# Performance work log

Hardware: AMD Instinct MI355X
Metric: run time of the kernel (lower is better)

The kernel has to match this reference:

```python
import jax, jax.numpy as jnp
import numpy as np

HIDDEN = 1024
HEADS = 16
HEAD_DIM = HIDDEN // HEADS


def setup_inputs() -> dict:
    key = jax.random.key(0)
    ks = jax.random.split(key, 7)
    B, S, H = 8, 1024, HIDDEN
    hidden_states = jax.random.normal(ks[0], (B, S, H), dtype=jnp.float32)
    attention_mask = jnp.zeros((B, 1, 1, S), dtype=jnp.float32)
    # Xavier-uniform weights [out, in], zero biases (matches module init)
    limit = float(np.sqrt(6.0 / (H + H)))
    Wq = jax.random.uniform(ks[1], (H, H), minval=-limit, maxval=limit, dtype=jnp.float32)
    Wk = jax.random.uniform(ks[2], (H, H), minval=-limit, maxval=limit, dtype=jnp.float32)
    Wv = jax.random.uniform(ks[3], (H, H), minval=-limit, maxval=limit, dtype=jnp.float32)
    bq = jnp.zeros((H,), dtype=jnp.float32)
    bk = jnp.zeros((H,), dtype=jnp.float32)
    bv = jnp.zeros((H,), dtype=jnp.float32)
    return {"hidden_states": hidden_states, "attention_mask": attention_mask,
            "Wq": Wq, "bq": bq, "Wk": Wk, "bk": bk, "Wv": Wv, "bv": bv}


def _split_heads(x):
    # [B, S, H] -> [B, heads, S, head_dim]
    B, S, _ = x.shape
    return x.reshape(B, S, HEADS, HEAD_DIM).transpose(0, 2, 1, 3)


def reference(hidden_states, attention_mask, Wq, bq, Wk, bk, Wv, bv):
    # Linear projections: y = x @ W^T + b  (weights stored [out, in] as in torch)
    q = _split_heads(hidden_states @ Wq.T + bq)
    k = _split_heads(hidden_states @ Wk.T + bk)
    v = _split_heads(hidden_states @ Wv.T + bv)
    scale = 1.0 / (HEAD_DIM ** 0.5)
    scores = jnp.einsum('bhqd,bhkd->bhqk', q, k) * scale  # [B,heads,S,S]
    scores = scores + attention_mask
    probs = jax.nn.softmax(scores, axis=-1)
    # dropout is identity at inference
    ctx = jnp.einsum('bhqk,bhkd->bhqd', probs, v)
    B, _, S, _ = ctx.shape
    return ctx.transpose(0, 2, 1, 3).reshape(B, S, HIDDEN)
```

## Files before the change

### kernel.cpp

```cpp
#include <hip/hip_runtime.h>
#include <hip/hip_bf16.h>
#include <stdint.h>

#define B_ 8
#define S_ 1024
#define NH_ 16
#define D_ 64
#define H_ 1024
#define M_TOT (B_*S_)
#define LOG2E 1.44269504088896f

typedef __attribute__((ext_vector_type(8))) short short8;
typedef __attribute__((ext_vector_type(4))) float f32x4;
typedef __attribute__((ext_vector_type(16))) float f32x16;

#if __has_builtin(__builtin_amdgcn_exp2f)
#define EXP2(x) __builtin_amdgcn_exp2f(x)
#else
#define EXP2(x) __expf((x) * 0.69314718056f)
#endif

static __device__ __forceinline__ unsigned short f2bf(float f) {
  union { float f; unsigned u; } c; c.f = f;
  unsigned u = c.u;
  return (unsigned short)((u + 0x7fffu + ((u >> 16) & 1u)) >> 16);
}

static __device__ __forceinline__ void gld_lds16(void* lds, const void* g) {
  __builtin_amdgcn_global_load_lds((const __attribute__((address_space(1))) unsigned*)g,
                                   (__attribute__((address_space(3))) unsigned*)lds, 16, 0, 0);
}

__global__ void cvt_f32_bf16(const float* __restrict__ X,
                             const float* __restrict__ Wq,
                             const float* __restrict__ Wk,
                             const float* __restrict__ Wv,
                             unsigned short* __restrict__ Xbf,
                             unsigned short* __restrict__ Wbf) {
  const long long NX = (long long)M_TOT * H_;
  const long long NW = (long long)H_ * H_;
  long long t = (long long)blockIdx.x * blockDim.x + threadIdx.x;
  const long long stride = (long long)gridDim.x * blockDim.x;
  const long long total4 = (NX + 3 * NW) >> 2;
  for (; t < total4; t += stride) {
    long long e = t << 2;
    const float* src; unsigned short* dst;
    if (e < NX) { src = X + e; dst = Xbf + e; }
    else {
      long long r = e - NX;
      int w = (int)(r / NW);
      long long o = r - (long long)w * NW;
      src = (w == 0 ? Wq : (w == 1 ? Wk : Wv)) + o;
      dst = Wbf + (long long)w * NW + o;
    }
    float4 v = *(const float4*)src;
    ushort4 u;
    u.x = f2bf(v.x); u.y = f2bf(v.y); u.z = f2bf(v.z); u.w = f2bf(v.w);
    *(ushort4*)dst = u;
  }
}

#define GBM 128
#define GBN 128
#define GBK 64

__global__ __launch_bounds__(256) void qkv_gemm(
    const unsigned short* __restrict__ Xbf,
    const unsigned short* __restrict__ Wbf,
    const float* __restrict__ bq, const float* __restrict__ bk,
    const float* __restrict__ bv,
    unsigned short* __restrict__ Qo, unsigned short* __restrict__ Ko,
    unsigned short* __restrict__ Vt) {
  __shared__ char lds[GBM * GBK * 2 * 2];
  char* ldsA = lds;
  char* ldsB = lds + GBM * GBK * 2;

  const int tid = threadIdx.x;
  const int w = tid >> 6;
  const int l = tid & 63;
  const int z = blockIdx.z;
  const int mtile = blockIdx.x * GBM;
  const int ntile = blockIdx.y * GBN;
  const int wm = w >> 1, wn = w & 1;
  const int lrow = l & 15, lgrp = l >> 4;

  const unsigned short* Wz = Wbf + (long long)z * H_ * H_;

  f32x4 acc[4][4];
  f32x4 zero = {0.f, 0.f, 0.f, 0.f};
  #pragma unroll
  for (int i = 0; i < 4; ++i)
    #pragma unroll
    for (int j = 0; j < 4; ++j) acc[i][j] = zero;

  for (int kt = 0; kt < H_ / GBK; ++kt) {
    const int k0 = kt * GBK;
    #pragma unroll
    for (int t = 0; t < 4; ++t) {
      int j = w * 4 + t;
      int row = j * 8 + (l >> 3);
      int so = ((l & 7) ^ (row & 7)) * 8;
      gld_lds16(ldsA + j * 1024, Xbf + (long long)(mtile + row) * H_ + k0 + so);
      gld_lds16(ldsB + j * 1024, Wz  + (long long)(ntile + row) * H_ + k0 + so);
    }
    __syncthreads();

    char* srcA = (z == 2) ? ldsB : ldsA;
    char* srcB = (z == 2) ? ldsA : ldsB;
    const int wA = (z == 2) ? wn : wm;
    const int wB = (z == 2) ? wm : wn;

    short8 af[4][2], bf[4][2];
    #pragma unroll
    for (int ib = 0; ib < 4; ++ib)
      #pragma unroll
      for (int ks = 0; ks < 2; ++ks) {
        int rA = wA * 64 + ib * 16 + lrow;
        af[ib][ks] = *(const short8*)(srcA + rA * 128 + (((ks * 4 + lgrp) ^ (rA & 7)) * 16));
        int rB = wB * 64 + ib * 16 + lrow;
        bf[ib][ks] = *(const short8*)(srcB + rB * 128 + (((ks * 4 + lgrp) ^ (rB & 7)) * 16));
      }
    #pragma unroll
    for (int ib = 0; ib < 4; ++ib)
      #pragma unroll
      for (int jb = 0; jb < 4; ++jb)
        #pragma unroll
        for (int ks = 0; ks < 2; ++ks)
          acc[ib][jb] = __builtin_amdgcn_mfma_f32_16x16x32_bf16(
              af[ib][ks], bf[jb][ks], acc[ib][jb], 0, 0, 0);
    __syncthreads();
  }

  const float* bias = (z == 0) ? bq : (z == 1) ? bk : bv;
  if (z != 2) {
    unsigned short* O = (z == 0) ? Qo : Ko;
    #pragma unroll
    for (int jb = 0; jb < 4; ++jb) {
      int n = ntile + wn * 64 + jb * 16 + lrow;
      float bv_ = bias[n];
      int h = n >> 6, d = n & 63;
      #pragma unroll
      for (int ib = 0; ib < 4; ++ib)
        #pragma unroll
        for (int r = 0; r < 4; ++r) {
          int m = mtile + wm * 64 + ib * 16 + lgrp * 4 + r;
          float val = acc[ib][jb][r] + bv_;
          if (z == 0) val *= 0.125f * LOG2E;
          int b = m >> 10, s = m & 1023;
          O[(((long long)(b * NH_ + h)) * S_ + s) * D_ + d] = f2bf(val);
        }
    }
  } else {
    #pragma unroll
    for (int ib = 0; ib < 4; ++ib)
      #pragma unroll
      for (int r = 0; r < 4; ++r) {
        int n = ntile + wn * 64 + ib * 16 + lgrp * 4 + r;
        float bv_ = bias[n];
        int h = n >> 6, d = n & 63;
        #pragma unroll
        for (int jb = 0; jb < 4; ++jb) {
          int m = mtile + wm * 64 + jb * 16 + lrow;
          float val = acc[ib][jb][r] + bv_;
          int b = m >> 10, s = m & 1023;
          Vt[(((long long)(b * NH_ + h)) * D_ + d) * S_ + s] = f2bf(val);
        }
      }
  }
}

__global__ __launch_bounds__(256, 2) void attn_fused(
    const unsigned short* __restrict__ Qbf,
    const unsigned short* __restrict__ Kbf,
    const unsigned short* __restrict__ Vtb,
    const float* __restrict__ mask,
    float* __restrict__ out) {
  __shared__ char lds[32768];
  const int tid = threadIdx.x, w = tid >> 6, l = tid & 63;
  const int l31 = l & 31, h = l >> 5;

  const int lid = blockIdx.x;
  const int xcd = lid & 7, k8 = lid >> 3;
  const int bh = xcd * 16 + (k8 >> 2);
  const int qt = k8 & 3;
  const int b = bh >> 4, hd = bh & 15;
  const int q0 = qt * 256 + w * 64;

  const unsigned short* Kg = Kbf + (long long)bh * S_ * D_;
  const unsigned short* Vg = Vtb + (long long)bh * D_ * S_;
  const float* mrow = mask + b * S_;

  {
    const int row = (w * 2) * 8 + (l >> 3);
    const int row1 = (w * 2 + 1) * 8 + (l >> 3);
    const int so = ((l & 7) ^ (row & 7)) * 8;
    const int so1 = ((l & 7) ^ (row1 & 7)) * 8;
    gld_lds16(lds + (w * 2) * 1024,        Kg + (long long)row * D_ + so);
    gld_lds16(lds + (w * 2 + 1) * 1024,    Kg + (long long)row1 * D_ + so1);
    gld_lds16(lds + 8192 + (w * 2) * 1024, Vg + (long long)row * S_ + so);
    gld_lds16(lds + 8192 + (w * 2 + 1) * 1024, Vg + (long long)row1 * S_ + so1);
  }

  short8 qf[2][4];
  #pragma unroll
  for (int qb = 0; qb < 2; ++qb)
    #pragma unroll
    for (int ks = 0; ks < 4; ++ks)
      qf[qb][ks] = *(const short8*)(Qbf + ((long long)bh * S_ + q0 + qb * 32 + l31) * D_ + ks * 16 + 8 * h);

  f32x16 acc[2][2];
  #pragma unroll
  for (int db = 0; db < 2; ++db)
    #pragma unroll
    for (int qb = 0; qb < 2; ++qb)
      #pragma unroll
      for (int r = 0; r < 16; ++r) acc[db][qb][r] = 0.f;
  float m_run[2] = {-1e30f, -1e30f};
  float l_run[2] = {0.f, 0.f};

  __syncthreads();

  for (int kt = 0; kt < S_ / 64; ++kt) {
    const int p = kt & 1;
    char* ldsK = lds + p * 16384;
    char* ldsV = ldsK + 8192;
    const int key0 = kt * 64;

    if (kt < S_ / 64 - 1) {
      char* nb = lds + (p ^ 1) * 16384;
      const int nk0 = key0 + 64;
      #pragma unroll
      for (int t = 0; t < 2; ++t) {
        int j = w * 2 + t;
        int row = j * 8 + (l >> 3);
        int so = ((l & 7) ^ (row & 7)) * 8;
        gld_lds16(nb + j * 1024,        Kg + (long long)(nk0 + row) * D_ + so);
        gld_lds16(nb + 8192 + j * 1024, Vg + (long long)row * S_ + nk0 + so);
      }
    }

    f32x16 sc[2][2];
    #pragma unroll
    for (int kb = 0; kb < 2; ++kb)
      #pragma unroll
      for (int qb = 0; qb < 2; ++qb)
        #pragma unroll
        for (int r = 0; r < 16; ++r) sc[kb][qb][r] = 0.f;

    #pragma unroll
    for (int kb = 0; kb < 2; ++kb) {
      short8 kf[4];
      #pragma unroll
      for (int ks = 0; ks < 4; ++ks) {
        int row = kb * 32 + l31;
        int g = (2 * ks + h) ^ (row & 7);
        kf[ks] = *(const short8*)(ldsK + row * 128 + g * 16);
      }
      __builtin_amdgcn_s_setprio(1);
      #pragma unroll
      for (int qb = 0; qb < 2; ++qb)
        #pragma unroll
        for (int ks = 0; ks < 4; ++ks)
          sc[kb][qb] = __builtin_amdgcn_mfma_f32_32x32x16_bf16(
              kf[ks], qf[qb][ks], sc[kb][qb], 0, 0, 0);
      __builtin_amdgcn_s_setprio(0);
    }

    short8 pfrag[2][4];
    #pragma unroll
    for (int qb = 0; qb < 2; ++qb) {
      float sv[32];
      #pragma unroll
      for (int kb = 0; kb < 2; ++kb)
        #pragma unroll
        for (int rg = 0; rg < 4; ++rg) {
          f32x4 m4 = *(const f32x4*)(mrow + key0 + kb * 32 + rg * 8 + 4 * h);
          #pragma unroll
          for (int c = 0; c < 4; ++c)
            sv[kb * 16 + rg * 4 + c] = fmaf(m4[c], LOG2E, sc[kb][qb][rg * 4 + c]);
        }
      float r16[16];
      #pragma unroll
      for (int i = 0; i < 16; ++i) r16[i] = fmaxf(sv[i], sv[i + 16]);
      #pragma unroll
      for (int i = 0; i < 8; ++i) r16[i] = fmaxf(r16[i], r16[i + 8]);
      #pragma unroll
      for (int i = 0; i < 4; ++i) r16[i] = fmaxf(r16[i], r16[i + 4]);
      float pm = fmaxf(fmaxf(r16[0], r16[1]), fmaxf(r16[2], r16[3]));
      pm = fmaxf(pm, __shfl_xor(pm, 32));
      if (!__all(pm - m_run[qb] <= 11.5f)) {
        float mn = fmaxf(m_run[qb], pm);
        float rs = EXP2(m_run[qb] - mn);
        m_run[qb] = mn;
        l_run[qb] *= rs;
        #pragma unroll
        for (int db = 0; db < 2; ++db)
          #pragma unroll
          for (int r = 0; r < 16; ++r) acc[db][qb][r] *= rs;
      }
      const float mcur = m_run[qb];
      #pragma unroll
      for (int i = 0; i < 32; ++i) sv[i] = EXP2(sv[i] - mcur);
      #pragma unroll
      for (int i = 0; i < 16; ++i) r16[i] = sv[i] + sv[i + 16];
      #pragma unroll
      for (int i = 0; i < 8; ++i) r16[i] = r16[i] + r16[i + 8];
      #pragma unroll
      for (int i = 0; i < 4; ++i) r16[i] = r16[i] + r16[i + 4];
      float ps = (r16[0] + r16[1]) + (r16[2] + r16[3]);
      ps += __shfl_xor(ps, 32);
      l_run[qb] += ps;

      unsigned Wd[8][2];
      #pragma unroll
      for (int j = 0; j < 8; ++j) {
        int base = (j >> 2) * 16 + (j & 3) * 4;
        asm("v_cvt_pk_bf16_f32 %0, %1, %2" : "=v"(Wd[j][0]) : "v"(sv[base + 0]), "v"(sv[base + 1]));
        asm("v_cvt_pk_bf16_f32 %0, %1, %2" : "=v"(Wd[j][1]) : "v"(sv[base + 2]), "v"(sv[base + 3]));
      }
      #pragma unroll
      for (int ks = 0; ks < 4; ++ks) {
        unsigned s0 = h ? Wd[2 * ks][0] : Wd[2 * ks + 1][0];
        unsigned s1 = h ? Wd[2 * ks][1] : Wd[2 * ks + 1][1];
        unsigned r0 = __shfl_xor(s0, 32);
        unsigned r1 = __shfl_xor(s1, 32);
        unsigned o0 = h ? Wd[2 * ks + 1][0] : Wd[2 * ks][0];
        unsigned o1 = h ? Wd[2 * ks + 1][1] : Wd[2 * ks][1];
        union { unsigned u[4]; short8 s; } fu;
        fu.u[0] = h ? r0 : o0;
        fu.u[1] = h ? r1 : o1;
        fu.u[2] = h ? o0 : r0;
        fu.u[3] = h ? o1 : r1;
        pfrag[qb][ks] = fu.s;
      }
    }

    #pragma unroll
    for (int db = 0; db < 2; ++db) {
      short8 vf[4];
      #pragma unroll
      for (int ks = 0; ks < 4; ++ks) {
        int row = db * 32 + l31;
        int g = (2 * ks + h) ^ (row & 7);
        vf[ks] = *(const short8*)(ldsV + row * 128 + g * 16);
      }
      __builtin_amdgcn_s_setprio(1);
      #pragma unroll
      for (int qb = 0; qb < 2; ++qb)
        #pragma unroll
        for (int ks = 0; ks < 4; ++ks)
          acc[db][qb] = __builtin_amdgcn_mfma_f32_32x32x16_bf16(
              vf[ks], pfrag[qb][ks], acc[db][qb], 0, 0, 0);
      __builtin_amdgcn_s_setprio(0);
    }

    __syncthreads();
  }

  #pragma unroll
  for (int qb = 0; qb < 2; ++qb) {
    float inv = 1.0f / l_run[qb];
    int q = q0 + qb * 32 + l31;
    float* orow = out + ((long long)b * S_ + q) * H_ + hd * D_;
    #pragma unroll
    for (int db = 0; db < 2; ++db)
      #pragma unroll
      for (int rg = 0; rg < 4; ++rg) {
        f32x4 v4;
        #pragma unroll
        for (int c = 0; c < 4; ++c) v4[c] = acc[db][qb][rg * 4 + c] * inv;
        *(f32x4*)(orow + db * 32 + rg * 8 + 4 * h) = v4;
      }
  }
}

extern "C" void kernel_launch(void* const* d_in, const int* in_sizes, int n_in,
                              void* d_out, int out_size, void* d_ws, size_t ws_size,
                              hipStream_t stream) {
  const float* X    = (const float*)d_in[0];
  const float* mask = (const float*)d_in[1];
  const float* Wq   = (const float*)d_in[2];
  const float* bq   = (const float*)d_in[3];
  const float* Wk   = (const float*)d_in[4];
  const float* bk   = (const float*)d_in[5];
  const float* Wv   = (const float*)d_in[6];
  const float* bv   = (const float*)d_in[7];
  float* out = (float*)d_out;

  char* ws = (char*)d_ws;
  unsigned short* Xbf = (unsigned short*)ws;
  unsigned short* Wbf = (unsigned short*)(ws + 16777216);
  unsigned short* Qb  = (unsigned short*)(ws + 23068672);
  unsigned short* Kb  = (unsigned short*)(ws + 39845888);
  unsigned short* Vt  = (unsigned short*)(ws + 56623104);

  hipLaunchKernelGGL(cvt_f32_bf16, dim3(2048), dim3(256), 0, stream,
                     X, Wq, Wk, Wv, Xbf, Wbf);
  hipLaunchKernelGGL(qkv_gemm, dim3(M_TOT / GBM, H_ / GBN, 3), dim3(256), 0, stream,
                     Xbf, Wbf, bq, bk, bv, Qb, Kb, Vt);
  hipLaunchKernelGGL(attn_fused, dim3(512), dim3(256), 0, stream,
                     Qb, Kb, Vt, mask, out);
}
```

Baseline: 138.0 us.

## Rewrite QKV GEMM with 256x128 tiles, triple-buffered LDS pipeline and XCD-aware grid

The QKV projection GEMM now uses 512-thread blocks on 256x128 tiles. Global-to-LDS loads go through a three-stage ring buffer, so tile k+2 is fetched while tile k is computed, and each k-step is split into four MFMA quadrants with explicit barriers, waitcnts and setprio. The 1D grid is remapped so consecutive blocks on the same XCD share N/z tiles, aiming for better L2 reuse. The goal is to hide load latency and cut per-iteration syncthreads stalls, at the cost of 144KB of LDS, which limits occupancy, and fragile hand-written vmcnt counting.

```diff
diff --git a/kernel.cpp b/kernel.cpp
--- a/kernel.cpp
+++ b/kernel.cpp
@@ -30,6 +30,11 @@
   __builtin_amdgcn_global_load_lds((const __attribute__((address_space(1))) unsigned*)g,
                                    (__attribute__((address_space(3))) unsigned*)lds, 16, 0, 0);
 }
+
+#define WAIT_LGKM0() asm volatile("s_waitcnt lgkmcnt(0)" ::: "memory")
+#define WAIT_VM(n)   asm volatile("s_waitcnt vmcnt(" #n ")" ::: "memory")
+#define SBAR()       __builtin_amdgcn_s_barrier()
+#define SCHED0()     __builtin_amdgcn_sched_barrier(0)
 
 __global__ void cvt_f32_bf16(const float* __restrict__ X,
                              const float* __restrict__ Wq,
@@ -60,31 +65,60 @@
   }
 }
 
-#define GBM 128
-#define GBN 128
-#define GBK 64
-
-__global__ __launch_bounds__(256) void qkv_gemm(
+#define QBM 256
+#define QBN 128
+#define QBK 64
+#define BUFSZ 49152
+
+__global__ __launch_bounds__(512, 2) void qkv_gemm(
     const unsigned short* __restrict__ Xbf,
     const unsigned short* __restrict__ Wbf,
     const float* __restrict__ bq, const float* __restrict__ bk,
     const float* __restrict__ bv,
     unsigned short* __restrict__ Qo, unsigned short* __restrict__ Ko,
     unsigned short* __restrict__ Vt) {
-  __shared__ char lds[GBM * GBK * 2 * 2];
-  char* ldsA = lds;
-  char* ldsB = lds + GBM * GBK * 2;
+  __shared__ char lds[3 * BUFSZ];
 
   const int tid = threadIdx.x;
   const int w = tid >> 6;
   const int l = tid & 63;
-  const int z = blockIdx.z;
-  const int mtile = blockIdx.x * GBM;
-  const int ntile = blockIdx.y * GBN;
+  const int lrow = l & 15, lgrp = l >> 4;
   const int wm = w >> 1, wn = w & 1;
-  const int lrow = l & 15, lgrp = l >> 4;
+
+  const int orig = blockIdx.x;
+  const int id = (orig & 7) * 96 + (orig >> 3);
+  const int mtile = (id & 31) * QBM;
+  const int rest = id >> 5;
+  const int ntile = (rest & 7) * QBN;
+  const int z = rest >> 3;
 
   const unsigned short* Wz = Wbf + (long long)z * H_ * H_;
+
+  const int srow = l >> 3;
+  const int sslot = l & 7;
+  auto stageA = [&](char* buf, int j, int k0) {
+    int row = j * 8 + srow;
+    int so = (sslot ^ (row & 7)) * 8;
+    gld_lds16(buf + j * 1024, Xbf + (long long)(mtile + row) * H_ + k0 + so);
+  };
+  auto stageB = [&](char* buf, int j, int k0) {
+    int row = j * 8 + srow;
+    int so = (sslot ^ (row & 7)) * 8;
+    gld_lds16(buf + 32768 + j * 1024, Wz + (long long)(ntile + row) * H_ + k0 + so);
+  };
+
+  const int strA = (z == 2 ? wn : wm) * 64;
+  const int strB = (z == 2 ? wm : wn) * 64;
+  const int offA = (z == 2) ? 32768 : 0;
+  const int offB = (z == 2) ? 0 : 32768;
+  auto rdA = [&](char* buf, int mh, int sub, int ks) -> short8 {
+    int r = strA + mh * 32 + sub * 16 + lrow;
+    return *(const short8*)(buf + offA + r * 128 + (((ks * 4 + lgrp) ^ (r & 7)) * 16));
+  };
+  auto rdB = [&](char* buf, int nh, int sub, int ks) -> short8 {
+    int r = strB + nh * 32 + sub * 16 + lrow;
+    return *(const short8*)(buf + offB + r * 128 + (((ks * 4 + lgrp) ^ (r & 7)) * 16));
+  };
 
   f32x4 acc[4][4];
   f32x4 zero = {0.f, 0.f, 0.f, 0.f};
@@ -93,58 +127,118 @@
     #pragma unroll
     for (int j = 0; j < 4; ++j) acc[i][j] = zero;
 
-  for (int kt = 0; kt < H_ / GBK; ++kt) {
-    const int k0 = kt * GBK;
-    #pragma unroll
-    for (int t = 0; t < 4; ++t) {
-      int j = w * 4 + t;
-      int row = j * 8 + (l >> 3);
-      int so = ((l & 7) ^ (row & 7)) * 8;
-      gld_lds16(ldsA + j * 1024, Xbf + (long long)(mtile + row) * H_ + k0 + so);
-      gld_lds16(ldsB + j * 1024, Wz  + (long long)(ntile + row) * H_ + k0 + so);
-    }
-    __syncthreads();
-
-    char* srcA = (z == 2) ? ldsB : ldsA;
-    char* srcB = (z == 2) ? ldsA : ldsB;
-    const int wA = (z == 2) ? wn : wm;
-    const int wB = (z == 2) ? wm : wn;
-
-    short8 af[4][2], bf[4][2];
-    #pragma unroll
-    for (int ib = 0; ib < 4; ++ib)
+  {
+    char* b0p = lds;
+    char* b1p = lds + BUFSZ;
+    #pragma unroll
+    for (int c = 0; c < 4; ++c) stageA(b0p, w * 4 + c, 0);
+    stageB(b0p, w * 2 + 0, 0); stageB(b0p, w * 2 + 1, 0);
+    #pragma unroll
+    for (int c = 0; c < 4; ++c) stageA(b1p, w * 4 + c, QBK);
+    stageB(b1p, w * 2 + 0, QBK); stageB(b1p, w * 2 + 1, QBK);
+  }
+  WAIT_VM(6);
+  SBAR();
+
+  #pragma unroll 1
+  for (int t = 0; t < 16; ++t) {
+    char* buf  = lds + (t % 3) * BUFSZ;
+    char* nbuf = lds + ((t + 2) % 3) * BUFSZ;
+    const int k0n = (t + 2) * QBK;
+    const bool st = (t + 2 < 16);
+
+    short8 af[2][2], b0[2][2], b1[2][2];
+
+    #pragma unroll
+    for (int sub = 0; sub < 2; ++sub)
       #pragma unroll
       for (int ks = 0; ks < 2; ++ks) {
-        int rA = wA * 64 + ib * 16 + lrow;
-        af[ib][ks] = *(const short8*)(srcA + rA * 128 + (((ks * 4 + lgrp) ^ (rA & 7)) * 16));
-        int rB = wB * 64 + ib * 16 + lrow;
-        bf[ib][ks] = *(const short8*)(srcB + rB * 128 + (((ks * 4 + lgrp) ^ (rB & 7)) * 16));
-      }
-    #pragma unroll
-    for (int ib = 0; ib < 4; ++ib)
-      #pragma unroll
-      for (int jb = 0; jb < 4; ++jb)
+        af[sub][ks] = rdA(buf, 0, sub, ks);
+        b0[sub][ks] = rdB(buf, 0, sub, ks);
+      }
+    if (st) { stageA(nbuf, w * 4 + 0, k0n); stageA(nbuf, w * 4 + 1, k0n); }
+    SBAR();
+    WAIT_LGKM0(); SCHED0();
+    __builtin_amdgcn_s_setprio(1);
+    #pragma unroll
+    for (int sa = 0; sa < 2; ++sa)
+      #pragma unroll
+      for (int sb = 0; sb < 2; ++sb)
         #pragma unroll
         for (int ks = 0; ks < 2; ++ks)
-          acc[ib][jb] = __builtin_amdgcn_mfma_f32_16x16x32_bf16(
-              af[ib][ks], bf[jb][ks], acc[ib][jb], 0, 0, 0);
-    __syncthreads();
+          acc[sa][sb] = __builtin_amdgcn_mfma_f32_16x16x32_bf16(
+              af[sa][ks], b0[sb][ks], acc[sa][sb], 0, 0, 0);
+    __builtin_amdgcn_s_setprio(0);
+    SBAR();
+
+    #pragma unroll
+    for (int sub = 0; sub < 2; ++sub)
+      #pragma unroll
+      for (int ks = 0; ks < 2; ++ks)
+        b1[sub][ks] = rdB(buf, 1, sub, ks);
+    if (st) { stageA(nbuf, w * 4 + 2, k0n); stageA(nbuf, w * 4 + 3, k0n); }
+    SBAR();
+    WAIT_LGKM0(); SCHED0();
+    __builtin_amdgcn_s_setprio(1);
+    #pragma unroll
+    for (int sa = 0; sa < 2; ++sa)
+      #pragma unroll
+      for (int sb = 0; sb < 2; ++sb)
+        #pragma unroll
+        for (int ks = 0; ks < 2; ++ks)
+          acc[sa][2 + sb] = __builtin_amdgcn_mfma_f32_16x16x32_bf16(
+              af[sa][ks], b1[sb][ks], acc[sa][2 + sb], 0, 0, 0);
+    __builtin_amdgcn_s_setprio(0);
+    SBAR();
+
+    #pragma unroll
+    for (int sub = 0; sub < 2; ++sub)
+      #pragma unroll
+      for (int ks = 0; ks < 2; ++ks)
+        af[sub][ks] = rdA(buf, 1, sub, ks);
+    if (st) { stageB(nbuf, w * 2 + 0, k0n); stageB(nbuf, w * 2 + 1, k0n); }
+    SBAR();
+    WAIT_LGKM0(); SCHED0();
+    __builtin_amdgcn_s_setprio(1);
+    #pragma unroll
+    for (int sa = 0; sa < 2; ++sa)
+      #pragma unroll
+      for (int sb = 0; sb < 2; ++sb)
+        #pragma unroll
+        for (int ks = 0; ks < 2; ++ks)
+          acc[2 + sa][2 + sb] = __builtin_amdgcn_mfma_f32_16x16x32_bf16(
+              af[sa][ks], b1[sb][ks], acc[2 + sa][2 + sb], 0, 0, 0);
+    __builtin_amdgcn_s_setprio(0);
+    SBAR();
+
+    __builtin_amdgcn_s_setprio(1);
+    #pragma unroll
+    for (int sa = 0; sa < 2; ++sa)
+      #pragma unroll
+      for (int sb = 0; sb < 2; ++sb)
+        #pragma unroll
+        for (int ks = 0; ks < 2; ++ks)
+          acc[2 + sa][sb] = __builtin_amdgcn_mfma_f32_16x16x32_bf16(
+              af[sa][ks], b0[sb][ks], acc[2 + sa][sb], 0, 0, 0);
+    __builtin_amdgcn_s_setprio(0);
+    if (t < 14) { WAIT_VM(6); } else { WAIT_VM(0); }
+    SBAR();
   }
 
   const float* bias = (z == 0) ? bq : (z == 1) ? bk : bv;
   if (z != 2) {
     unsigned short* O = (z == 0) ? Qo : Ko;
     #pragma unroll
-    for (int jb = 0; jb < 4; ++jb) {
-      int n = ntile + wn * 64 + jb * 16 + lrow;
+    for (int in = 0; in < 4; ++in) {
+      int n = ntile + wn * 64 + in * 16 + lrow;
       float bv_ = bias[n];
       int h = n >> 6, d = n & 63;
       #pragma unroll
-      for (int ib = 0; ib < 4; ++ib)
+      for (int im = 0; im < 4; ++im)
         #pragma unroll
         for (int r = 0; r < 4; ++r) {
-          int m = mtile + wm * 64 + ib * 16 + lgrp * 4 + r;
-          float val = acc[ib][jb][r] + bv_;
+          int m = mtile + wm * 64 + im * 16 + lgrp * 4 + r;
+          float val = acc[im][in][r] + bv_;
           if (z == 0) val *= 0.125f * LOG2E;
           int b = m >> 10, s = m & 1023;
           O[(((long long)(b * NH_ + h)) * S_ + s) * D_ + d] = f2bf(val);
@@ -152,17 +246,17 @@
     }
   } else {
     #pragma unroll
-    for (int ib = 0; ib < 4; ++ib)
+    for (int im = 0; im < 4; ++im)
       #pragma unroll
       for (int r = 0; r < 4; ++r) {
-        int n = ntile + wn * 64 + ib * 16 + lgrp * 4 + r;
-        float bv_ = bias[n];
-        int h = n >> 6, d = n & 63;
-        #pragma unroll
-        for (int jb = 0; jb < 4; ++jb) {
-          int m = mtile + wm * 64 + jb * 16 + lrow;
-          float val = acc[ib][jb][r] + bv_;
-          int b = m >> 10, s = m & 1023;
+        int nfull = ntile + wn * 64 + im * 16 + lgrp * 4 + r;
+        float bv_ = bias[nfull];
+        int h = nfull >> 6, d = nfull & 63;
+        #pragma unroll
+        for (int in = 0; in < 4; ++in) {
+          int mfull = mtile + wm * 64 + in * 16 + lrow;
+          float val = acc[im][in][r] + bv_;
+          int b = mfull >> 10, s = mfull & 1023;
           Vt[(((long long)(b * NH_ + h)) * D_ + d) * S_ + s] = f2bf(val);
         }
       }
@@ -396,7 +490,7 @@
 
   hipLaunchKernelGGL(cvt_f32_bf16, dim3(2048), dim3(256), 0, stream,
                      X, Wq, Wk, Wv, Xbf, Wbf);
-  hipLaunchKernelGGL(qkv_gemm, dim3(M_TOT / GBM, H_ / GBN, 3), dim3(256), 0, stream,
+  hipLaunchKernelGGL(qkv_gemm, dim3(768), dim3(512), 0, stream,
                      Xbf, Wbf, bq, bk, bv, Qb, Kb, Vt);
   hipLaunchKernelGGL(attn_fused, dim3(512), dim3(256), 0, stream,
                      Qb, Kb, Vt, mask, out);
```

New measurement: 146.0 us. 1.06x slower.
